# Kernel optimization log

Hardware: AMD Instinct MI355X
Metric: run time of the kernel (lower is better)

## Reference

```python
import jax, jax.numpy as jnp
import numpy as np

NUM_JOINTS = 17

def _build_norm_adj():
    # Same skeleton as _get_skeleton_edges, made bidirectional; row-normalized
    # so that A @ x computes the per-node mean over neighbors (every joint
    # has degree >= 1, matching the original's mean aggregation branch).
    conns = [(0, 7), (7, 8), (8, 9), (9, 10), (0, 1), (1, 2), (2, 3), (0, 4),
             (4, 5), (5, 6), (8, 11), (11, 12), (12, 13), (8, 14), (14, 15), (15, 16)]
    A = np.zeros((NUM_JOINTS, NUM_JOINTS), dtype=np.float32)
    for a, b in conns:
        A[a, b] = 1.0
        A[b, a] = 1.0
    deg = A.sum(axis=1, keepdims=True)
    A = A / np.maximum(deg, 1.0)
    return jnp.asarray(A)

def _xavier(key, out_dim, in_dim):
    lim = np.sqrt(6.0 / (in_dim + out_dim)).astype(np.float32)
    return jax.random.uniform(key, (out_dim, in_dim), jnp.float32, -lim, lim)

def setup_inputs() -> dict:
    key = jax.random.key(0)
    ks = jax.random.split(key, 6)
    B, J, D_IN, H, D_OUT = 65536, NUM_JOINTS, 3, 64, 256
    x = jax.random.normal(ks[0], (B, J, D_IN), jnp.float32)
    return {
        "x": x,
        "A": _build_norm_adj(),
        "W1": _xavier(ks[1], H, D_IN), "b1": jnp.zeros((H,), jnp.float32),
        "W2": _xavier(ks[2], H, H),    "b2": jnp.zeros((H,), jnp.float32),
        "W3": _xavier(ks[3], H, H),    "b3": jnp.zeros((H,), jnp.float32),
        "Wp1": _xavier(ks[4], H, J * H), "bp1": jnp.zeros((H,), jnp.float32),
        "Wp2": _xavier(ks[5], D_OUT, H), "bp2": jnp.zeros((D_OUT,), jnp.float32),
    }

def reference(x, A, W1, b1, W2, b2, W3, b3, Wp1, bp1, Wp2, bp2):
    # GCN layer 1: neighbor-mean aggregate then linear (+ReLU; dropout = eval identity)
    h = jnp.einsum('ij,bjd->bid', A, x)            # (B, 17, 3)
    h = jax.nn.relu(h @ W1.T + b1)                 # (B, 17, 64)
    # GCN layer 2
    h = jnp.einsum('ij,bjd->bid', A, h)
    h = jax.nn.relu(h @ W2.T + b2)
    # GCN layer 3 (no activation)
    h = jnp.einsum('ij,bjd->bid', A, h)
    h = h @ W3.T + b3                              # (B, 17, 64)
    # Global pool MLP over flattened joints
    flat = h.reshape(h.shape[0], -1)               # (B, 17*64)
    z = jax.nn.relu(flat @ Wp1.T + bp1)            # (B, 64)
    return z @ Wp2.T + bp2                         # (B, 256)
```

## Files before the change

kernel.cpp:

```cpp
#include <hip/hip_runtime.h>
#include <hip/hip_bf16.h>
#include <stdint.h>

typedef __attribute__((ext_vector_type(8))) short short8;
typedef __attribute__((ext_vector_type(4))) float f32x4;
typedef __attribute__((ext_vector_type(4))) unsigned int u32x4;
typedef __attribute__((ext_vector_type(2))) unsigned int u32x2;

constexpr int kNBR[17][4] = {
    {7, 1, 4, 0}, {0, 2, 0, 0}, {1, 3, 0, 0}, {2, 0, 0, 0},
    {0, 5, 0, 0}, {4, 6, 0, 0}, {5, 0, 0, 0}, {0, 8, 0, 0},
    {7, 9, 11, 14}, {8, 10, 0, 0}, {9, 0, 0, 0}, {8, 12, 0, 0},
    {11, 13, 0, 0}, {12, 0, 0, 0}, {8, 15, 0, 0}, {14, 16, 0, 0},
    {15, 0, 0, 0}};
constexpr int kDEG[17] = {3,2,2,1,2,2,1,2,4,2,1,2,2,1,2,2,1};
constexpr float kRDEG[5] = {0.f, 1.f, 0.5f, 0.33333334f, 0.25f};
constexpr int kWNT[4] = {3, 4, 5, 5};
constexpr int kWJT[4][5] = {{8, 1, 2, 0, 0},
                            {0, 4, 5, 3, 0},
                            {7, 9, 11, 6, 10},
                            {12, 14, 15, 13, 16}};

template <int N> struct IC { static constexpr int v = N; };

__device__ inline unsigned short f2bf(float f) {
  union { float f; uint32_t u; } v; v.f = f;
  uint32_t u = v.u;
  uint32_t r = u + 0x7fffu + ((u >> 16) & 1u);
  return (unsigned short)(r >> 16);
}
__device__ inline uint32_t pk2(float a, float b) {
  union { __hip_bfloat162 h; uint32_t u; } v;
  v.h = __float22bfloat162_rn(make_float2(a, b));
  return v.u;
}
__device__ inline f32x4 mfma16(short8 a, short8 b, f32x4 c) {
  return __builtin_amdgcn_mfma_f32_16x16x32_bf16(a, b, c, 0, 0, 0);
}

__global__ void prep(const float* __restrict__ W1,
                     const float* __restrict__ W2,
                     const float* __restrict__ Wp2,
                     const float* __restrict__ W3,
                     const float* __restrict__ Wp1,
                     const float* __restrict__ b3,
                     const float* __restrict__ bp1,
                     const float* __restrict__ b1,
                     short* __restrict__ W1b,
                     short* __restrict__ W2b,
                     short* __restrict__ Wp2b,
                     short* __restrict__ Mb,
                     float* __restrict__ bp1p) {
  __shared__ float w3s[4096];
  __shared__ float Qs[256];
  const int tid = threadIdx.x;
  const int bx = blockIdx.x;
  if (bx < 272) {
    for (int q = tid; q < 4096; q += 256) w3s[q] = W3[q];
    {
      int ro = tid >> 6, k = tid & 63;
      int r = bx * 4 + ro;
      int f = r / 17, i = r - f * 17;
      int dj = kDEG[i];
      float s = 0.f;
#pragma unroll
      for (int t = 0; t < 4; t++) {
        if (t < dj) {
          int nb = kNBR[i][t];
          s += kRDEG[kDEG[nb]] * Wp1[f * 1088 + nb * 64 + k];
        }
      }
      Qs[ro * 64 + k] = s;
    }
    __syncthreads();
    {
      int ro = tid >> 6, c = tid & 63;
      int r = bx * 4 + ro;
      int f = r / 17, i = r - f * 17;
      float s = 0.f;
#pragma unroll
      for (int k = 0; k < 64; k++) s += Qs[ro * 64 + k] * w3s[k * 64 + c];
      int col = i * 64 + c;
      int kk = col >> 5, qq = (col >> 3) & 3, cb = col & 7;
      int w = f >> 4, l15 = f & 15;
      Mb[(((w * 34 + kk) * 64) + qq * 16 + l15) * 8 + cb] = (short)f2bf(s);
    }
  } else if (bx < 354) {
    int q = (bx - 272) * 256 + tid;
    if (q < 4096) W2b[q] = (short)f2bf(W2[q]);
    int q2 = q - 4096;
    if (q2 >= 0 && q2 < 16384) Wp2b[q2] = (short)f2bf(Wp2[q2]);
    int q3 = q - 20480;
    if (q3 >= 0 && q3 < 512) {
      int k = q3 & 7, row = q3 >> 3;
      short v = 0;
      if (k < 3) v = (short)f2bf(W1[row * 3 + k]);
      else if (k == 3) v = (short)f2bf(b1[row]);
      W1b[q3] = v;
    }
  } else {
    int wv = tid >> 6, l = tid & 63;
    int f = (bx - 354) * 4 + wv;
    float s = 0.f;
#pragma unroll
    for (int i = 0; i < 17; i++) s += Wp1[f * 1088 + i * 64 + l] * b3[l];
#pragma unroll
    for (int off = 32; off > 0; off >>= 1) s += __shfl_down(s, off);
    if (l == 0) bp1p[f] = bp1[f] + s;
  }
}

__launch_bounds__(256, 2)
__global__ void gcn_main(const float* __restrict__ X,
                         const short* __restrict__ Mb,
                         const short* __restrict__ Wp2b,
                         const short* __restrict__ W2b,
                         const short* __restrict__ W1b,
                         const float* __restrict__ bp1p,
                         const float* __restrict__ b2g,
                         const float* __restrict__ bp2g,
                         float* __restrict__ OUT) {
  __shared__ __align__(16) short hbuf[2 * 272 * 64];
  __shared__ __align__(16) float xs[2 * 816];
  __shared__ __align__(16) float sbias[128];

  const int tid = threadIdx.x;
  const int wave = tid >> 6;
  const int lane = tid & 63;
  const int ln15 = lane & 15;
  const int quad = lane >> 4;
  const int bx = blockIdx.x;

  auto hswz = [](int row, int cb) { return row * 128 + (cb ^ ((row & 7) << 4)); };

  for (int q = tid; q < 408; q += 256)
    ((f32x4*)xs)[q] = ((const f32x4*)(X + (size_t)bx * 1632))[q];
  short8 w1f[4];
#pragma unroll
  for (int ft = 0; ft < 4; ft++)
    w1f[ft] = *(const short8*)(W1b + (ft * 16 + ln15) * 8);
  if (tid < 128) {
    sbias[tid] = (tid < 64) ? b2g[tid] : bp1p[tid - 64];
  }
  __syncthreads();

  f32x4 acc[2][5][4];

  auto l1 = [&](auto wv) {
    constexpr int WV = decltype(wv)::v;
    constexpr int NT = kWNT[WV];
#pragma unroll
    for (int t = 0; t < NT; t++) {
      const int j = kWJT[WV][t];
      const int dj = kDEG[j];
      const float w = kRDEG[dj];
      union { short8 s; u32x4 u; } fr[2];
#pragma unroll
      for (int g = 0; g < 2; g++) {
        const float* xsg = xs + g * 816;
        fr[g].u = (u32x4){0u, 0u, 0u, 0u};
        if (quad == 0) {
          float s0, s1, s2;
          {
            int b = ln15 * 51 + kNBR[j][0] * 3;
            s0 = xsg[b]; s1 = xsg[b + 1]; s2 = xsg[b + 2];
          }
          if (dj > 1) {
            int b = ln15 * 51 + kNBR[j][1] * 3;
            s0 += xsg[b]; s1 += xsg[b + 1]; s2 += xsg[b + 2];
          }
          if (dj > 2) {
            int b = ln15 * 51 + kNBR[j][2] * 3;
            s0 += xsg[b]; s1 += xsg[b + 1]; s2 += xsg[b + 2];
          }
          if (dj > 3) {
            int b = ln15 * 51 + kNBR[j][3] * 3;
            s0 += xsg[b]; s1 += xsg[b + 1]; s2 += xsg[b + 2];
          }
          fr[g].u.x = pk2(s0 * w, s1 * w);
          fr[g].u.y = pk2(s2 * w, 1.0f);
        }
      }
#pragma unroll
      for (int g = 0; g < 2; g++) {
        f32x4 a[4];
#pragma unroll
        for (int ft = 0; ft < 4; ft++)
          a[ft] = mfma16(w1f[ft], fr[g].s, (f32x4){0.f, 0.f, 0.f, 0.f});
#pragma unroll
        for (int ft = 0; ft < 4; ft++) {
          int fb = ft * 16 + quad * 4;
          u32x2 pk;
          pk.x = pk2(fmaxf(a[ft].x, 0.f), fmaxf(a[ft].y, 0.f));
          pk.y = pk2(fmaxf(a[ft].z, 0.f), fmaxf(a[ft].w, 0.f));
          *(u32x2*)((char*)hbuf + g * 34816 + hswz(j * 16 + ln15, fb * 2)) = pk;
        }
      }
    }
  };

  auto l2m = [&](auto wv) {
    constexpr int WV = decltype(wv)::v;
    constexpr int NT = kWNT[WV];
#pragma unroll
    for (int g = 0; g < 2; g++)
#pragma unroll
      for (int t = 0; t < NT; t++)
#pragma unroll
        for (int ft = 0; ft < 4; ft++)
          acc[g][t][ft] = (f32x4){0.f, 0.f, 0.f, 0.f};
#pragma unroll
    for (int kk = 0; kk < 2; kk++) {
      short8 w2f[4];
#pragma unroll
      for (int ft = 0; ft < 4; ft++)
        w2f[ft] = *(const short8*)(W2b + (ft * 16 + ln15) * 64 + kk * 32 + quad * 8);
#pragma unroll
      for (int t = 0; t < NT; t++) {
        const int j = kWJT[WV][t];
#pragma unroll
        for (int s = 0; s < 4; s++) {
          if (s < kDEG[j]) {
            const int i = kNBR[j][s];
#pragma unroll
            for (int g = 0; g < 2; g++) {
              short8 bf = *(const short8*)((char*)hbuf + g * 34816 +
                                           hswz(i * 16 + ln15, kk * 64 + quad * 16));
#pragma unroll
              for (int ft = 0; ft < 4; ft++)
                acc[g][t][ft] = mfma16(w2f[ft], bf, acc[g][t][ft]);
            }
          }
        }
      }
    }
  };

  auto l2wb = [&](auto wv) {
    constexpr int WV = decltype(wv)::v;
    constexpr int NT = kWNT[WV];
#pragma unroll
    for (int t = 0; t < NT; t++) {
      const int j = kWJT[WV][t];
      const float w = kRDEG[kDEG[j]];
#pragma unroll
      for (int g = 0; g < 2; g++)
#pragma unroll
        for (int ft = 0; ft < 4; ft++) {
          int fb = ft * 16 + quad * 4;
          f32x4 bv = *(const f32x4*)&sbias[fb];
          f32x4 c = acc[g][t][ft];
          u32x2 pk;
          pk.x = pk2(fmaxf(c.x * w + bv.x, 0.f), fmaxf(c.y * w + bv.y, 0.f));
          pk.y = pk2(fmaxf(c.z * w + bv.z, 0.f), fmaxf(c.w * w + bv.w, 0.f));
          *(u32x2*)((char*)hbuf + g * 34816 + hswz(j * 16 + ln15, fb * 2)) = pk;
        }
    }
  };

#define WDISPATCH(F)                       \
  do {                                     \
    if (wave == 0) F(IC<0>{});             \
    else if (wave == 1) F(IC<1>{});        \
    else if (wave == 2) F(IC<2>{});        \
    else F(IC<3>{});                       \
  } while (0)

  WDISPATCH(l1);
  __syncthreads();
  WDISPATCH(l2m);
  __syncthreads();

  const short8* mrow = ((const short8*)Mb) + (size_t)wave * 34 * 64 + lane;
  short8 pf[12];
#pragma unroll
  for (int p = 0; p < 12; p++) pf[p] = mrow[p * 64];

  WDISPATCH(l2wb);
  __syncthreads();
#undef WDISPATCH

  const int fbw = wave * 16 + quad * 4;
  f32x4 zcv[2];
  {
    f32x4 bvp = *(const f32x4*)&sbias[64 + fbw];
    f32x4 pacc[2][4];
#pragma unroll
    for (int g = 0; g < 2; g++) {
      pacc[g][0] = bvp;
      pacc[g][1] = (f32x4){0.f, 0.f, 0.f, 0.f};
      pacc[g][2] = (f32x4){0.f, 0.f, 0.f, 0.f};
      pacc[g][3] = (f32x4){0.f, 0.f, 0.f, 0.f};
    }
#pragma unroll
    for (int kk = 0; kk < 34; kk++) {
      short8 af = pf[kk % 12];
      if (kk + 12 < 34) pf[kk % 12] = mrow[(kk + 12) * 64];
      int i = kk >> 1;
#pragma unroll
      for (int g = 0; g < 2; g++) {
        short8 bf = *(const short8*)((char*)hbuf + g * 34816 +
                                     hswz(i * 16 + ln15, (kk & 1) * 64 + quad * 16));
        pacc[g][kk & 3] = mfma16(af, bf, pacc[g][kk & 3]);
      }
    }
    zcv[0] = (pacc[0][0] + pacc[0][1]) + (pacc[0][2] + pacc[0][3]);
    zcv[1] = (pacc[1][0] + pacc[1][1]) + (pacc[1][2] + pacc[1][3]);
  }
  short8 wp2f[4][2];
#pragma unroll
  for (int t = 0; t < 4; t++) {
    int ot = wave + 4 * t;
    wp2f[t][0] = *(const short8*)(Wp2b + (ot * 16 + ln15) * 64 + quad * 8);
    wp2f[t][1] = *(const short8*)(Wp2b + (ot * 16 + ln15) * 64 + 32 + quad * 8);
  }
#pragma unroll
  for (int g = 0; g < 2; g++) {
    char* zbB = (char*)(xs + g * 816);
    u32x2 pk;
    pk.x = pk2(fmaxf(zcv[g].x, 0.f), fmaxf(zcv[g].y, 0.f));
    pk.y = pk2(fmaxf(zcv[g].z, 0.f), fmaxf(zcv[g].w, 0.f));
    *(u32x2*)(zbB + hswz(ln15, fbw * 2)) = pk;
  }
  __syncthreads();

#pragma unroll
  for (int g = 0; g < 2; g++) {
    char* zbB = (char*)(xs + g * 816);
    short8 bf0 = *(const short8*)(zbB + hswz(ln15, quad * 16));
    short8 bf1 = *(const short8*)(zbB + hswz(ln15, 64 + quad * 16));
    int e0g = bx * 32 + g * 16;
#pragma unroll
    for (int t = 0; t < 4; t++) {
      int ot = wave + 4 * t;
      f32x4 a = (f32x4){0.f, 0.f, 0.f, 0.f};
      a = mfma16(wp2f[t][0], bf0, a);
      a = mfma16(wp2f[t][1], bf1, a);
      int ob = ot * 16 + quad * 4;
      f32x4 bv = *(const f32x4*)&bp2g[ob];
      f32x4 res = a + bv;
      *(f32x4*)(OUT + (size_t)(e0g + ln15) * 256 + ob) = res;
    }
  }
}

extern "C" void kernel_launch(void* const* d_in, const int* in_sizes, int n_in,
                              void* d_out, int out_size, void* d_ws, size_t ws_size,
                              hipStream_t stream) {
  const float* X = (const float*)d_in[0];
  const float* W1 = (const float*)d_in[2];
  const float* b1 = (const float*)d_in[3];
  const float* W2 = (const float*)d_in[4];
  const float* b2 = (const float*)d_in[5];
  const float* W3 = (const float*)d_in[6];
  const float* b3 = (const float*)d_in[7];
  const float* Wp1 = (const float*)d_in[8];
  const float* bp1 = (const float*)d_in[9];
  const float* Wp2 = (const float*)d_in[10];
  const float* bp2 = (const float*)d_in[11];
  float* OUT = (float*)d_out;
  const int B = in_sizes[0] / 51;

  char* ws = (char*)d_ws;
  short* Mb = (short*)(ws + 0);
  short* Wp2b = (short*)(ws + 139264);
  short* W2b = (short*)(ws + 172032);
  short* W1b = (short*)(ws + 180224);
  float* bp1p = (float*)(ws + 181248);

  prep<<<370, 256, 0, stream>>>(W1, W2, Wp2, W3, Wp1, b3, bp1, b1,
                                W1b, W2b, Wp2b, Mb, bp1p);
  gcn_main<<<B / 32, 256, 0, stream>>>(X, Mb, Wp2b, W2b, W1b, bp1p,
                                       b2, bp2, OUT);
}
```

Measured before the change: 173.8 us.

## Specialize whole per-wave body as template, shrinking layer-2 accumulator live range

Replaces the per-phase wave dispatch with one templated per-wave function that runs every phase, so each wave compiles as a single straight-line specialized path with barriers inside the branches. Layer 2 now finishes each joint/group accumulation and packs it to bf16 right away, keeping packed results instead of the full fp32 accumulator array. W2 fragments are loaded once for both k halves, and the Wp1 prefetch depth drops from 12 to 8. The goal is lower register pressure and fewer spills at two blocks per CU. Calling __syncthreads inside divergent per-wave branches depends on every wave reaching matching barriers.

```diff
diff --git a/kernel.cpp b/kernel.cpp
--- a/kernel.cpp
+++ b/kernel.cpp
@@ -21,8 +21,6 @@
                             {7, 9, 11, 6, 10},
                             {12, 14, 15, 13, 16}};
 
-template <int N> struct IC { static constexpr int v = N; };
-
 __device__ inline unsigned short f2bf(float f) {
   union { float f; uint32_t u; } v; v.f = f;
   uint32_t u = v.u;
@@ -36,6 +34,9 @@
 }
 __device__ inline f32x4 mfma16(short8 a, short8 b, f32x4 c) {
   return __builtin_amdgcn_mfma_f32_16x16x32_bf16(a, b, c, 0, 0, 0);
+}
+__device__ inline int hswz(int row, int cb) {
+  return row * 128 + (cb ^ ((row & 7) << 4));
 }
 
 __global__ void prep(const float* __restrict__ W1,
@@ -110,6 +111,189 @@
   }
 }
 
+template <int WV>
+__device__ __forceinline__ void waveBody(
+    const short* __restrict__ Mb, const short* __restrict__ Wp2b,
+    const short* __restrict__ W2b, const float* __restrict__ bp2g,
+    float* __restrict__ OUT, short* hbuf, float* xs, float* sbias,
+    const short8 (&w1f)[4], int bx, int lane, int ln15, int quad) {
+  constexpr int NT = kWNT[WV];
+  char* hb0 = (char*)hbuf;
+
+#pragma unroll
+  for (int t = 0; t < NT; t++) {
+    const int j = kWJT[WV][t];
+    const int dj = kDEG[j];
+    const float w = kRDEG[dj];
+    union { short8 s; u32x4 u; } fr[2];
+#pragma unroll
+    for (int g = 0; g < 2; g++) {
+      const float* xsg = xs + g * 816;
+      fr[g].u = (u32x4){0u, 0u, 0u, 0u};
+      if (quad == 0) {
+        float s0, s1, s2;
+        {
+          int b = ln15 * 51 + kNBR[j][0] * 3;
+          s0 = xsg[b]; s1 = xsg[b + 1]; s2 = xsg[b + 2];
+        }
+        if (dj > 1) {
+          int b = ln15 * 51 + kNBR[j][1] * 3;
+          s0 += xsg[b]; s1 += xsg[b + 1]; s2 += xsg[b + 2];
+        }
+        if (dj > 2) {
+          int b = ln15 * 51 + kNBR[j][2] * 3;
+          s0 += xsg[b]; s1 += xsg[b + 1]; s2 += xsg[b + 2];
+        }
+        if (dj > 3) {
+          int b = ln15 * 51 + kNBR[j][3] * 3;
+          s0 += xsg[b]; s1 += xsg[b + 1]; s2 += xsg[b + 2];
+        }
+        fr[g].u.x = pk2(s0 * w, s1 * w);
+        fr[g].u.y = pk2(s2 * w, 1.0f);
+      }
+    }
+#pragma unroll
+    for (int g = 0; g < 2; g++) {
+      f32x4 a[4];
+#pragma unroll
+      for (int ft = 0; ft < 4; ft++)
+        a[ft] = mfma16(w1f[ft], fr[g].s, (f32x4){0.f, 0.f, 0.f, 0.f});
+#pragma unroll
+      for (int ft = 0; ft < 4; ft++) {
+        int fb = ft * 16 + quad * 4;
+        u32x2 pk;
+        pk.x = pk2(fmaxf(a[ft].x, 0.f), fmaxf(a[ft].y, 0.f));
+        pk.y = pk2(fmaxf(a[ft].z, 0.f), fmaxf(a[ft].w, 0.f));
+        *(u32x2*)(hb0 + g * 34816 + hswz(j * 16 + ln15, fb * 2)) = pk;
+      }
+    }
+  }
+  __syncthreads();
+
+  short8 w2f[2][4];
+#pragma unroll
+  for (int kk = 0; kk < 2; kk++)
+#pragma unroll
+    for (int ft = 0; ft < 4; ft++)
+      w2f[kk][ft] = *(const short8*)(W2b + (ft * 16 + ln15) * 64 + kk * 32 + quad * 8);
+
+  u32x2 pkh2[2][NT][4];
+#pragma unroll
+  for (int t = 0; t < NT; t++) {
+    const int j = kWJT[WV][t];
+    const int dj = kDEG[j];
+    const float w = kRDEG[dj];
+#pragma unroll
+    for (int g = 0; g < 2; g++) {
+      f32x4 a[4];
+#pragma unroll
+      for (int ft = 0; ft < 4; ft++) a[ft] = (f32x4){0.f, 0.f, 0.f, 0.f};
+#pragma unroll
+      for (int kk = 0; kk < 2; kk++)
+#pragma unroll
+        for (int s = 0; s < 4; s++)
+          if (s < dj) {
+            const int i = kNBR[j][s];
+            short8 bf = *(const short8*)(hb0 + g * 34816 +
+                                         hswz(i * 16 + ln15, kk * 64 + quad * 16));
+#pragma unroll
+            for (int ft = 0; ft < 4; ft++)
+              a[ft] = mfma16(w2f[kk][ft], bf, a[ft]);
+          }
+#pragma unroll
+      for (int ft = 0; ft < 4; ft++) {
+        int fb = ft * 16 + quad * 4;
+        f32x4 bv = *(const f32x4*)&sbias[fb];
+        u32x2 pk;
+        pk.x = pk2(fmaxf(a[ft].x * w + bv.x, 0.f), fmaxf(a[ft].y * w + bv.y, 0.f));
+        pk.y = pk2(fmaxf(a[ft].z * w + bv.z, 0.f), fmaxf(a[ft].w * w + bv.w, 0.f));
+        pkh2[g][t][ft] = pk;
+      }
+    }
+  }
+  const short8* mrow = ((const short8*)Mb) + (size_t)WV * 34 * 64 + lane;
+  short8 pf[8];
+#pragma unroll
+  for (int p = 0; p < 8; p++) pf[p] = mrow[p * 64];
+  __syncthreads();
+
+#pragma unroll
+  for (int t = 0; t < NT; t++) {
+    const int j = kWJT[WV][t];
+#pragma unroll
+    for (int g = 0; g < 2; g++)
+#pragma unroll
+      for (int ft = 0; ft < 4; ft++) {
+        int fb = ft * 16 + quad * 4;
+        *(u32x2*)(hb0 + g * 34816 + hswz(j * 16 + ln15, fb * 2)) = pkh2[g][t][ft];
+      }
+  }
+  __syncthreads();
+
+  const int fbw = WV * 16 + quad * 4;
+  f32x4 zcv[2];
+  {
+    f32x4 bvp = *(const f32x4*)&sbias[64 + fbw];
+    f32x4 pacc[2][4];
+#pragma unroll
+    for (int g = 0; g < 2; g++) {
+      pacc[g][0] = bvp;
+      pacc[g][1] = (f32x4){0.f, 0.f, 0.f, 0.f};
+      pacc[g][2] = (f32x4){0.f, 0.f, 0.f, 0.f};
+      pacc[g][3] = (f32x4){0.f, 0.f, 0.f, 0.f};
+    }
+#pragma unroll
+    for (int kk = 0; kk < 34; kk++) {
+      short8 af = pf[kk & 7];
+      if (kk + 8 < 34) pf[kk & 7] = mrow[(kk + 8) * 64];
+      int i = kk >> 1;
+#pragma unroll
+      for (int g = 0; g < 2; g++) {
+        short8 bf = *(const short8*)(hb0 + g * 34816 +
+                                     hswz(i * 16 + ln15, (kk & 1) * 64 + quad * 16));
+        pacc[g][kk & 3] = mfma16(af, bf, pacc[g][kk & 3]);
+      }
+    }
+    zcv[0] = (pacc[0][0] + pacc[0][1]) + (pacc[0][2] + pacc[0][3]);
+    zcv[1] = (pacc[1][0] + pacc[1][1]) + (pacc[1][2] + pacc[1][3]);
+  }
+  short8 wp2f[4][2];
+#pragma unroll
+  for (int t = 0; t < 4; t++) {
+    int ot = WV + 4 * t;
+    wp2f[t][0] = *(const short8*)(Wp2b + (ot * 16 + ln15) * 64 + quad * 8);
+    wp2f[t][1] = *(const short8*)(Wp2b + (ot * 16 + ln15) * 64 + 32 + quad * 8);
+  }
+#pragma unroll
+  for (int g = 0; g < 2; g++) {
+    char* zbB = (char*)(xs + g * 816);
+    u32x2 pk;
+    pk.x = pk2(fmaxf(zcv[g].x, 0.f), fmaxf(zcv[g].y, 0.f));
+    pk.y = pk2(fmaxf(zcv[g].z, 0.f), fmaxf(zcv[g].w, 0.f));
+    *(u32x2*)(zbB + hswz(ln15, fbw * 2)) = pk;
+  }
+  __syncthreads();
+
+#pragma unroll
+  for (int g = 0; g < 2; g++) {
+    char* zbB = (char*)(xs + g * 816);
+    short8 bf0 = *(const short8*)(zbB + hswz(ln15, quad * 16));
+    short8 bf1 = *(const short8*)(zbB + hswz(ln15, 64 + quad * 16));
+    int e0g = bx * 32 + g * 16;
+#pragma unroll
+    for (int t = 0; t < 4; t++) {
+      int ot = WV + 4 * t;
+      f32x4 a = (f32x4){0.f, 0.f, 0.f, 0.f};
+      a = mfma16(wp2f[t][0], bf0, a);
+      a = mfma16(wp2f[t][1], bf1, a);
+      int ob = ot * 16 + quad * 4;
+      f32x4 bv = *(const f32x4*)&bp2g[ob];
+      f32x4 res = a + bv;
+      *(f32x4*)(OUT + (size_t)(e0g + ln15) * 256 + ob) = res;
+    }
+  }
+}
+
 __launch_bounds__(256, 2)
 __global__ void gcn_main(const float* __restrict__ X,
                          const short* __restrict__ Mb,
@@ -131,8 +315,6 @@
   const int quad = lane >> 4;
   const int bx = blockIdx.x;
 
-  auto hswz = [](int row, int cb) { return row * 128 + (cb ^ ((row & 7) << 4)); };
-
   for (int q = tid; q < 408; q += 256)
     ((f32x4*)xs)[q] = ((const f32x4*)(X + (size_t)bx * 1632))[q];
   short8 w1f[4];
@@ -144,204 +326,14 @@
   }
   __syncthreads();
 
-  f32x4 acc[2][5][4];
-
-  auto l1 = [&](auto wv) {
-    constexpr int WV = decltype(wv)::v;
-    constexpr int NT = kWNT[WV];
-#pragma unroll
-    for (int t = 0; t < NT; t++) {
-      const int j = kWJT[WV][t];
-      const int dj = kDEG[j];
-      const float w = kRDEG[dj];
-      union { short8 s; u32x4 u; } fr[2];
-#pragma unroll
-      for (int g = 0; g < 2; g++) {
-        const float* xsg = xs + g * 816;
-        fr[g].u = (u32x4){0u, 0u, 0u, 0u};
-        if (quad == 0) {
-          float s0, s1, s2;
-          {
-            int b = ln15 * 51 + kNBR[j][0] * 3;
-            s0 = xsg[b]; s1 = xsg[b + 1]; s2 = xsg[b + 2];
-          }
-          if (dj > 1) {
-            int b = ln15 * 51 + kNBR[j][1] * 3;
-            s0 += xsg[b]; s1 += xsg[b + 1]; s2 += xsg[b + 2];
-          }
-          if (dj > 2) {
-            int b = ln15 * 51 + kNBR[j][2] * 3;
-            s0 += xsg[b]; s1 += xsg[b + 1]; s2 += xsg[b + 2];
-          }
-          if (dj > 3) {
-            int b = ln15 * 51 + kNBR[j][3] * 3;
-            s0 += xsg[b]; s1 += xsg[b + 1]; s2 += xsg[b + 2];
-          }
-          fr[g].u.x = pk2(s0 * w, s1 * w);
-          fr[g].u.y = pk2(s2 * w, 1.0f);
-        }
-      }
-#pragma unroll
-      for (int g = 0; g < 2; g++) {
-        f32x4 a[4];
-#pragma unroll
-        for (int ft = 0; ft < 4; ft++)
-          a[ft] = mfma16(w1f[ft], fr[g].s, (f32x4){0.f, 0.f, 0.f, 0.f});
-#pragma unroll
-        for (int ft = 0; ft < 4; ft++) {
-          int fb = ft * 16 + quad * 4;
-          u32x2 pk;
-          pk.x = pk2(fmaxf(a[ft].x, 0.f), fmaxf(a[ft].y, 0.f));
-          pk.y = pk2(fmaxf(a[ft].z, 0.f), fmaxf(a[ft].w, 0.f));
-          *(u32x2*)((char*)hbuf + g * 34816 + hswz(j * 16 + ln15, fb * 2)) = pk;
-        }
-      }
-    }
-  };
-
-  auto l2m = [&](auto wv) {
-    constexpr int WV = decltype(wv)::v;
-    constexpr int NT = kWNT[WV];
-#pragma unroll
-    for (int g = 0; g < 2; g++)
-#pragma unroll
-      for (int t = 0; t < NT; t++)
-#pragma unroll
-        for (int ft = 0; ft < 4; ft++)
-          acc[g][t][ft] = (f32x4){0.f, 0.f, 0.f, 0.f};
-#pragma unroll
-    for (int kk = 0; kk < 2; kk++) {
-      short8 w2f[4];
-#pragma unroll
-      for (int ft = 0; ft < 4; ft++)
-        w2f[ft] = *(const short8*)(W2b + (ft * 16 + ln15) * 64 + kk * 32 + quad * 8);
-#pragma unroll
-      for (int t = 0; t < NT; t++) {
-        const int j = kWJT[WV][t];
-#pragma unroll
-        for (int s = 0; s < 4; s++) {
-          if (s < kDEG[j]) {
-            const int i = kNBR[j][s];
-#pragma unroll
-            for (int g = 0; g < 2; g++) {
-              short8 bf = *(const short8*)((char*)hbuf + g * 34816 +
-                                           hswz(i * 16 + ln15, kk * 64 + quad * 16));
-#pragma unroll
-              for (int ft = 0; ft < 4; ft++)
-                acc[g][t][ft] = mfma16(w2f[ft], bf, acc[g][t][ft]);
-            }
-          }
-        }
-      }
-    }
-  };
-
-  auto l2wb = [&](auto wv) {
-    constexpr int WV = decltype(wv)::v;
-    constexpr int NT = kWNT[WV];
-#pragma unroll
-    for (int t = 0; t < NT; t++) {
-      const int j = kWJT[WV][t];
-      const float w = kRDEG[kDEG[j]];
-#pragma unroll
-      for (int g = 0; g < 2; g++)
-#pragma unroll
-        for (int ft = 0; ft < 4; ft++) {
-          int fb = ft * 16 + quad * 4;
-          f32x4 bv = *(const f32x4*)&sbias[fb];
-          f32x4 c = acc[g][t][ft];
-          u32x2 pk;
-          pk.x = pk2(fmaxf(c.x * w + bv.x, 0.f), fmaxf(c.y * w + bv.y, 0.f));
-          pk.y = pk2(fmaxf(c.z * w + bv.z, 0.f), fmaxf(c.w * w + bv.w, 0.f));
-          *(u32x2*)((char*)hbuf + g * 34816 + hswz(j * 16 + ln15, fb * 2)) = pk;
-        }
-    }
-  };
-
-#define WDISPATCH(F)                       \
-  do {                                     \
-    if (wave == 0) F(IC<0>{});             \
-    else if (wave == 1) F(IC<1>{});        \
-    else if (wave == 2) F(IC<2>{});        \
-    else F(IC<3>{});                       \
-  } while (0)
-
-  WDISPATCH(l1);
-  __syncthreads();
-  WDISPATCH(l2m);
-  __syncthreads();
-
-  const short8* mrow = ((const short8*)Mb) + (size_t)wave * 34 * 64 + lane;
-  short8 pf[12];
-#pragma unroll
-  for (int p = 0; p < 12; p++) pf[p] = mrow[p * 64];
-
-  WDISPATCH(l2wb);
-  __syncthreads();
-#undef WDISPATCH
-
-  const int fbw = wave * 16 + quad * 4;
-  f32x4 zcv[2];
-  {
-    f32x4 bvp = *(const f32x4*)&sbias[64 + fbw];
-    f32x4 pacc[2][4];
-#pragma unroll
-    for (int g = 0; g < 2; g++) {
-      pacc[g][0] = bvp;
-      pacc[g][1] = (f32x4){0.f, 0.f, 0.f, 0.f};
-      pacc[g][2] = (f32x4){0.f, 0.f, 0.f, 0.f};
-      pacc[g][3] = (f32x4){0.f, 0.f, 0.f, 0.f};
-    }
-#pragma unroll
-    for (int kk = 0; kk < 34; kk++) {
-      short8 af = pf[kk % 12];
-      if (kk + 12 < 34) pf[kk % 12] = mrow[(kk + 12) * 64];
-      int i = kk >> 1;
-#pragma unroll
-      for (int g = 0; g < 2; g++) {
-        short8 bf = *(const short8*)((char*)hbuf + g * 34816 +
-                                     hswz(i * 16 + ln15, (kk & 1) * 64 + quad * 16));
-        pacc[g][kk & 3] = mfma16(af, bf, pacc[g][kk & 3]);
-      }
-    }
-    zcv[0] = (pacc[0][0] + pacc[0][1]) + (pacc[0][2] + pacc[0][3]);
-    zcv[1] = (pacc[1][0] + pacc[1][1]) + (pacc[1][2] + pacc[1][3]);
-  }
-  short8 wp2f[4][2];
-#pragma unroll
-  for (int t = 0; t < 4; t++) {
-    int ot = wave + 4 * t;
-    wp2f[t][0] = *(const short8*)(Wp2b + (ot * 16 + ln15) * 64 + quad * 8);
-    wp2f[t][1] = *(const short8*)(Wp2b + (ot * 16 + ln15) * 64 + 32 + quad * 8);
-  }
-#pragma unroll
-  for (int g = 0; g < 2; g++) {
-    char* zbB = (char*)(xs + g * 816);
-    u32x2 pk;
-    pk.x = pk2(fmaxf(zcv[g].x, 0.f), fmaxf(zcv[g].y, 0.f));
-    pk.y = pk2(fmaxf(zcv[g].z, 0.f), fmaxf(zcv[g].w, 0.f));
-    *(u32x2*)(zbB + hswz(ln15, fbw * 2)) = pk;
-  }
-  __syncthreads();
-
-#pragma unroll
-  for (int g = 0; g < 2; g++) {
-    char* zbB = (char*)(xs + g * 816);
-    short8 bf0 = *(const short8*)(zbB + hswz(ln15, quad * 16));
-    short8 bf1 = *(const short8*)(zbB + hswz(ln15, 64 + quad * 16));
-    int e0g = bx * 32 + g * 16;
-#pragma unroll
-    for (int t = 0; t < 4; t++) {
-      int ot = wave + 4 * t;
-      f32x4 a = (f32x4){0.f, 0.f, 0.f, 0.f};
-      a = mfma16(wp2f[t][0], bf0, a);
-      a = mfma16(wp2f[t][1], bf1, a);
-      int ob = ot * 16 + quad * 4;
-      f32x4 bv = *(const f32x4*)&bp2g[ob];
-      f32x4 res = a + bv;
-      *(f32x4*)(OUT + (size_t)(e0g + ln15) * 256 + ob) = res;
-    }
-  }
+  if (wave == 0)
+    waveBody<0>(Mb, Wp2b, W2b, bp2g, OUT, hbuf, xs, sbias, w1f, bx, lane, ln15, quad);
+  else if (wave == 1)
+    waveBody<1>(Mb, Wp2b, W2b, bp2g, OUT, hbuf, xs, sbias, w1f, bx, lane, ln15, quad);
+  else if (wave == 2)
+    waveBody<2>(Mb, Wp2b, W2b, bp2g, OUT, hbuf, xs, sbias, w1f, bx, lane, ln15, quad);
+  else
+    waveBody<3>(Mb, Wp2b, W2b, bp2g, OUT, hbuf, xs, sbias, w1f, bx, lane, ln15, quad);
 }
 
 extern "C" void kernel_launch(void* const* d_in, const int* in_sizes, int n_in,
```

Result: faster. 155.2 us (-10.7%).
